# Kernel tuning notes

Hardware: AMD Instinct MI355X
Metric: run time of the kernel (lower is better)

Reference implementation:

```python
import jax, jax.numpy as jnp
import numpy as np

B, T, F, D, H, L = 4, 1024, 128, 512, 8, 4
DFF = 4 * D
NE, MD = 16, 20
HD = D // H
SCALE = 1.0 / HD ** 0.5


def _ln(x, w, b):
    m = jnp.mean(x, axis=-1, keepdims=True)
    v = jnp.mean((x - m) ** 2, axis=-1, keepdims=True)
    return (x - m) * jax.lax.rsqrt(v + 1e-5) * w + b


def setup_inputs() -> dict:
    key = jax.random.key(0)
    ks = jax.random.split(key, 16)
    rn = lambda k, shape: jax.random.normal(k, shape, jnp.float32) * 0.02
    return {
        'node_features': jax.random.normal(ks[0], (B, T, F), jnp.float32),
        'centrality': jax.random.uniform(ks[1], (B, T), jnp.float32),
        'edge_types': jax.random.randint(ks[2], (B, T, T), 0, NE),
        'sp_dist': jax.random.randint(ks[3], (B, T, T), 0, MD + 1),
        'node_W': rn(ks[4], (F, D)), 'node_b': jnp.zeros((D,), jnp.float32),
        'cent_W': rn(ks[5], (D,)), 'cent_b': jnp.zeros((D,), jnp.float32),
        'edge_emb': rn(ks[6], (NE, H)), 'dist_emb': rn(ks[7], (MD + 1, H)),
        'ln1_w': jnp.ones((L, D), jnp.float32), 'ln1_b': jnp.zeros((L, D), jnp.float32),
        'q_W': rn(ks[8], (L, D, D)), 'q_b': jnp.zeros((L, D), jnp.float32),
        'k_W': rn(ks[9], (L, D, D)), 'k_b': jnp.zeros((L, D), jnp.float32),
        'v_W': rn(ks[10], (L, D, D)), 'v_b': jnp.zeros((L, D), jnp.float32),
        'o_W': rn(ks[11], (L, D, D)), 'o_b': jnp.zeros((L, D), jnp.float32),
        'ln2_w': jnp.ones((L, D), jnp.float32), 'ln2_b': jnp.zeros((L, D), jnp.float32),
        'f1_W': rn(ks[12], (L, D, DFF)), 'f1_b': jnp.zeros((L, DFF), jnp.float32),
        'f2_W': rn(ks[13], (L, DFF, D)), 'f2_b': jnp.zeros((L, D), jnp.float32),
    }


def _forward(node_features, centrality, edge_types, sp_dist,
             node_W, node_b, cent_W, cent_b, edge_emb, dist_emb,
             ln1_w, ln1_b, q_W, q_b, k_W, k_b, v_W, v_b, o_W, o_b,
             ln2_w, ln2_b, f1_W, f1_b, f2_W, f2_b):
    # node embedding + centrality encoding
    h = node_features @ node_W + node_b                      # [B,T,D]
    h = h + centrality[..., None] * cent_W + cent_b          # Linear(1,D)
    # Graphormer attention bias: [B,T,T,H] -> [B,H,T,T]
    sp = jnp.clip(sp_dist, 0, MD)
    attn_bias = (edge_emb[edge_types] + dist_emb[sp]).transpose(0, 3, 1, 2)

    def step(h, p):
        l1w, l1b, qW, qb, kW, kb, vW, vb, oW, ob, l2w, l2b, w1, b1, w2, b2 = p
        x = _ln(h, l1w, l1b)
        q = (x @ qW + qb).reshape(B, T, H, HD)
        k = (x @ kW + kb).reshape(B, T, H, HD)
        v = (x @ vW + vb).reshape(B, T, H, HD)
        scores = jnp.einsum('bihd,bjhd->bhij', q, k) * SCALE + attn_bias
        attn = jax.nn.softmax(scores, axis=-1)
        o = jnp.einsum('bhij,bjhd->bihd', attn, v).reshape(B, T, D)
        h = h + (o @ oW + ob)                                # dropout in eval mode
        x2 = _ln(h, l2w, l2b)
        h = h + (jax.nn.silu(x2 @ w1 + b1) @ w2 + b2)
        return h, None

    layer_params = (ln1_w, ln1_b, q_W, q_b, k_W, k_b, v_W, v_b, o_W, o_b,
                    ln2_w, ln2_b, f1_W, f1_b, f2_W, f2_b)
    h, _ = jax.lax.scan(step, h, layer_params)
    return h


def reference(node_features, centrality, edge_types, sp_dist,
              node_W, node_b, cent_W, cent_b, edge_emb, dist_emb,
              ln1_w, ln1_b, q_W, q_b, k_W, k_b, v_W, v_b, o_W, o_b,
              ln2_w, ln2_b, f1_W, f1_b, f2_W, f2_b):
    return _forward(node_features, centrality, edge_types, sp_dist,
                    node_W, node_b, cent_W, cent_b, edge_emb, dist_emb,
                    ln1_w, ln1_b, q_W, q_b, k_W, k_b, v_W, v_b, o_W, o_b,
                    ln2_w, ln2_b, f1_W, f1_b, f2_W, f2_b)
```

## Files before the change

kernel.cpp:

```cpp
#include <hip/hip_runtime.h>
#include <cstddef>
#include <cstdint>

#define B_    4
#define T_    1024
#define F_    128
#define D_    512
#define H_    8
#define L_    4
#define DFF_  2048
#define HD_   64
#define SCALE_ 0.125f

typedef __attribute__((ext_vector_type(8))) short bf16x8;
typedef __attribute__((ext_vector_type(4))) float f32x4;

#define AS1(p) ((const __attribute__((address_space(1))) void*)(p))
#define AS3(p) ((__attribute__((address_space(3))) void*)(p))

__device__ __forceinline__ short f2bf(float f) {
    unsigned u = __float_as_uint(f);
    u += 0x7FFFu + ((u >> 16) & 1u);
    return (short)(u >> 16);
}

__global__ __launch_bounds__(256) void cast_nf_k(
    const float* __restrict__ src, short* __restrict__ dst)
{
    const int i = (blockIdx.x * 256 + threadIdx.x) << 2;
    const float4 v = *(const float4*)(src + i);
    short4 o = make_short4(f2bf(v.x), f2bf(v.y), f2bf(v.z), f2bf(v.w));
    *(short4*)(dst + i) = o;
}

__global__ __launch_bounds__(256) void ln_k(
    const float* __restrict__ X, const float* __restrict__ w,
    const float* __restrict__ b, short* __restrict__ Y)
{
    const int row = blockIdx.x;
    const int tid = threadIdx.x;
    const float* xr = X + (size_t)row * D_;
    const float v0 = xr[tid];
    const float v1 = xr[tid + 256];
    float s  = v0 + v1;
    float s2 = v0 * v0 + v1 * v1;
#pragma unroll
    for (int off = 1; off < 64; off <<= 1) {
        s  += __shfl_xor(s,  off);
        s2 += __shfl_xor(s2, off);
    }
    __shared__ float ss[4], ss2[4];
    if ((tid & 63) == 0) { ss[tid >> 6] = s; ss2[tid >> 6] = s2; }
    __syncthreads();
    s  = ss[0]  + ss[1]  + ss[2]  + ss[3];
    s2 = ss2[0] + ss2[1] + ss2[2] + ss2[3];
    const float mean = s * (1.f / D_);
    const float var  = s2 * (1.f / D_) - mean * mean;
    const float r    = rsqrtf(var + 1e-5f);
    short* yr = Y + (size_t)row * D_;
    yr[tid]       = f2bf((v0 - mean) * r * w[tid]       + b[tid]);
    yr[tid + 256] = f2bf((v1 - mean) * r * w[tid + 256] + b[tid + 256]);
}

__global__ __launch_bounds__(256) void transpose_all_k(
    const float* __restrict__ qW, const float* __restrict__ kW,
    const float* __restrict__ vW, const float* __restrict__ oW,
    const float* __restrict__ f1W, const float* __restrict__ f2W,
    const float* __restrict__ nW,
    short* __restrict__ WqkvT, short* __restrict__ WoT,
    short* __restrict__ Wf1T, short* __restrict__ Wf2T,
    short* __restrict__ nWt)
{
    const int id = blockIdx.y;
    const float* src; short* dst; int K, N;
    if (id < 12) {
        const int l = id / 3, which = id % 3;
        const float* s3 = (which == 0) ? qW : (which == 1) ? kW : vW;
        src = s3 + (size_t)l * D_ * D_;
        dst = WqkvT + ((size_t)l * 3 + which) * D_ * D_;
        K = D_; N = D_;
    } else if (id < 16) {
        const int l = id - 12;
        src = oW + (size_t)l * D_ * D_;  dst = WoT + (size_t)l * D_ * D_;
        K = D_; N = D_;
    } else if (id < 20) {
        const int l = id - 16;
        src = f1W + (size_t)l * D_ * DFF_;  dst = Wf1T + (size_t)l * DFF_ * D_;
        K = D_; N = DFF_;
    } else if (id < 24) {
        const int l = id - 20;
        src = f2W + (size_t)l * DFF_ * D_;  dst = Wf2T + (size_t)l * D_ * DFF_;
        K = DFF_; N = D_;
    } else {
        src = nW; dst = nWt; K = F_; N = D_;
    }
    const int ntiles = (K >> 5) * (N >> 5);
    if ((int)blockIdx.x >= ntiles) return;
    const int nt = N >> 5;
    const int k0 = (blockIdx.x / nt) << 5, n0 = (blockIdx.x % nt) << 5;

    __shared__ float t[32][33];
    const int c = threadIdx.x, r0 = threadIdx.y;
#pragma unroll
    for (int i = 0; i < 32; i += 8)
        t[r0 + i][c] = src[(size_t)(k0 + r0 + i) * N + n0 + c];
    __syncthreads();
#pragma unroll
    for (int i = 0; i < 32; i += 8)
        dst[(size_t)(n0 + r0 + i) * K + k0 + c] = f2bf(t[c][r0 + i]);
}

__global__ __launch_bounds__(256) void fuse_bias_k(
    const float* __restrict__ qb, const float* __restrict__ kb,
    const float* __restrict__ vb, float* __restrict__ dst)
{
    const int i = blockIdx.x * 256 + threadIdx.x;
    const int l = i / 1536, c = i % 1536;
    float v;
    if (c < 512)       v = qb[l * 512 + c];
    else if (c < 1024) v = kb[l * 512 + c - 512];
    else               v = vb[l * 512 + c - 1024];
    dst[i] = v;
}

__global__ __launch_bounds__(256) void bias_k(
    const int* __restrict__ et, const int* __restrict__ sp,
    const float* __restrict__ ee, const float* __restrict__ de,
    short* __restrict__ biasT)
{
    __shared__ float eeS[16][8], deS[21][8];
    const int tid = threadIdx.x;
    if (tid < 128) eeS[tid >> 3][tid & 7] = ee[tid];
    for (int t = tid; t < 168; t += 256)
        deS[t >> 3][t & 7] = de[t];
    __syncthreads();
    const int gid = blockIdx.x * 256 + tid;
    const int j4  = (gid & 255) << 2;
    const int bi  = gid >> 8;
    const size_t base = (size_t)bi * T_ + j4;
    const int4 e = *(const int4*)(et + base);
    const int4 s = *(const int4*)(sp + base);
    const int b = bi >> 10, i = bi & 1023;
    const int ex[4] = {e.x, e.y, e.z, e.w};
    const int sx[4] = {min(s.x, 20), min(s.y, 20), min(s.z, 20), min(s.w, 20)};
#pragma unroll
    for (int h = 0; h < 8; ++h) {
        short4 o;
        o.x = f2bf(eeS[ex[0]][h] + deS[sx[0]][h]);
        o.y = f2bf(eeS[ex[1]][h] + deS[sx[1]][h]);
        o.z = f2bf(eeS[ex[2]][h] + deS[sx[2]][h]);
        o.w = f2bf(eeS[ex[3]][h] + deS[sx[3]][h]);
        *(short4*)(biasT + ((size_t)((b * H_ + h) * T_ + i)) * T_ + j4) = o;
    }
}

__global__ __launch_bounds__(256) void embed_mm_k(
    const short* __restrict__ A, const short* __restrict__ Wt,
    const float* __restrict__ nb, const float* __restrict__ cb,
    const float* __restrict__ cW, const float* __restrict__ cent,
    float* __restrict__ C)
{
    const int K = F_, N = D_;
    __shared__ short As[128 * 32];
    __shared__ short Bs[64 * 32];
    const int tid  = threadIdx.x;
    const int lane = tid & 63, wv = tid >> 6;
    const int bm = blockIdx.y << 7, bn = blockIdx.x << 6;
    const int wm = (wv & 1) << 6, wn = (wv >> 1) << 5;

    const int c0 = (wv << 6) + lane;
    const int m0 = c0 >> 2, q0 = (c0 & 3) ^ ((m0 >> 1) & 3);
    const int c1 = 256 + c0;
    const int m1 = c1 >> 2, q1 = (c1 & 3) ^ ((m1 >> 1) & 3);

    const short* gA0 = A  + (size_t)(bm + m0) * K + (q0 << 3);
    const short* gA1 = A  + (size_t)(bm + m1) * K + (q1 << 3);
    const short* gB0 = Wt + (size_t)(bn + m0) * K + (q0 << 3);

    f32x4 acc[4][2];
#pragma unroll
    for (int i = 0; i < 4; ++i)
#pragma unroll
        for (int j = 0; j < 2; ++j)
            acc[i][j] = (f32x4){0.f, 0.f, 0.f, 0.f};

    const int fm = lane & 15, fq = lane >> 4;
    int caddr[4], baddr[2];
#pragma unroll
    for (int t = 0; t < 4; ++t) {
        const int rowA = wm + (t << 4) + fm;
        caddr[t] = ((rowA << 2) + (fq ^ ((rowA >> 1) & 3))) << 3;
    }
#pragma unroll
    for (int t = 0; t < 2; ++t) {
        const int rowB = wn + (t << 4) + fm;
        baddr[t] = ((rowB << 2) + (fq ^ ((rowB >> 1) & 3))) << 3;
    }

    for (int k0 = 0; k0 < K; k0 += 32) {
        __builtin_amdgcn_global_load_lds(AS1(gA0), AS3(As + (wv << 9)),        16, 0, 0);
        __builtin_amdgcn_global_load_lds(AS1(gA1), AS3(As + 2048 + (wv << 9)), 16, 0, 0);
        __builtin_amdgcn_global_load_lds(AS1(gB0), AS3(Bs + (wv << 9)),        16, 0, 0);
        gA0 += 32; gA1 += 32; gB0 += 32;
        __syncthreads();

        bf16x8 af[4], bf[2];
#pragma unroll
        for (int t = 0; t < 4; ++t) af[t] = *(const bf16x8*)(As + caddr[t]);
#pragma unroll
        for (int t = 0; t < 2; ++t) bf[t] = *(const bf16x8*)(Bs + baddr[t]);
#pragma unroll
        for (int i = 0; i < 4; ++i)
#pragma unroll
            for (int j = 0; j < 2; ++j)
                acc[i][j] = __builtin_amdgcn_mfma_f32_16x16x32_bf16(
                    af[i], bf[j], acc[i][j], 0, 0, 0);
        __syncthreads();
    }

    const int col0 = bn + wn + fm;
    const int row0 = bm + wm + (fq << 2);
#pragma unroll
    for (int j = 0; j < 2; ++j) {
        const int colg = col0 + (j << 4);
        const float bb = nb[colg] + cb[colg];
        const float cw = cW[colg];
#pragma unroll
        for (int i = 0; i < 4; ++i) {
#pragma unroll
            for (int r = 0; r < 4; ++r) {
                const int rowg = row0 + (i << 4) + r;
                C[(size_t)rowg * N + colg] = acc[i][j][r] + bb + cent[rowg] * cw;
            }
        }
    }
}

template <int OUTM, int ACT, int RES>
__global__ __launch_bounds__(256) void mm_k(
    const short* __restrict__ A, const short* __restrict__ Wt,
    const float* __restrict__ bias, const float* __restrict__ R,
    void* __restrict__ Cv, short* __restrict__ VtOut, int M, int N, int K)
{
    __shared__ short As[128 * 32];
    __shared__ short Bs[128 * 32];
    const int tid  = threadIdx.x;
    const int lane = tid & 63, wv = tid >> 6;
    const int bm = blockIdx.y << 7, bn = blockIdx.x << 7;
    const int wm = (wv & 1) << 6, wn = (wv >> 1) << 6;

    const int c0 = (wv << 6) + lane;
    const int m0 = c0 >> 2, q0 = (c0 & 3) ^ ((m0 >> 1) & 3);
    const int c1 = 256 + c0;
    const int m1 = c1 >> 2, q1 = (c1 & 3) ^ ((m1 >> 1) & 3);

    const short* gA0 = A  + (size_t)(bm + m0) * K + (q0 << 3);
    const short* gA1 = A  + (size_t)(bm + m1) * K + (q1 << 3);
    const short* gB0 = Wt + (size_t)(bn + m0) * K + (q0 << 3);
    const short* gB1 = Wt + (size_t)(bn + m1) * K + (q1 << 3);

    f32x4 acc[4][4];
#pragma unroll
    for (int i = 0; i < 4; ++i)
#pragma unroll
        for (int j = 0; j < 4; ++j)
            acc[i][j] = (f32x4){0.f, 0.f, 0.f, 0.f};

    const int fm = lane & 15, fq = lane >> 4;
    int caddr[4], baddr[4];
#pragma unroll
    for (int t = 0; t < 4; ++t) {
        const int rowA = wm + (t << 4) + fm;
        caddr[t] = ((rowA << 2) + (fq ^ ((rowA >> 1) & 3))) << 3;
        const int rowB = wn + (t << 4) + fm;
        baddr[t] = ((rowB << 2) + (fq ^ ((rowB >> 1) & 3))) << 3;
    }

    for (int k0 = 0; k0 < K; k0 += 32) {
        __builtin_amdgcn_global_load_lds(AS1(gA0), AS3(As + (wv << 9)),        16, 0, 0);
        __builtin_amdgcn_global_load_lds(AS1(gA1), AS3(As + 2048 + (wv << 9)), 16, 0, 0);
        __builtin_amdgcn_global_load_lds(AS1(gB0), AS3(Bs + (wv << 9)),        16, 0, 0);
        __builtin_amdgcn_global_load_lds(AS1(gB1), AS3(Bs + 2048 + (wv << 9)), 16, 0, 0);
        gA0 += 32; gA1 += 32; gB0 += 32; gB1 += 32;
        __syncthreads();

        bf16x8 af[4], bf[4];
#pragma unroll
        for (int t = 0; t < 4; ++t) {
            af[t] = *(const bf16x8*)(As + caddr[t]);
            bf[t] = *(const bf16x8*)(Bs + baddr[t]);
        }
#pragma unroll
        for (int i = 0; i < 4; ++i)
#pragma unroll
            for (int j = 0; j < 4; ++j)
                acc[i][j] = __builtin_amdgcn_mfma_f32_16x16x32_bf16(
                    af[i], bf[j], acc[i][j], 0, 0, 0);
        __syncthreads();
    }

    const int col0 = bn + wn + fm;
    const int row0 = bm + wm + (fq << 2);
    float* Cf = (float*)Cv;
    short* Cb = (short*)Cv;
#pragma unroll
    for (int j = 0; j < 4; ++j) {
        const int colg = col0 + (j << 4);
        const float bb = bias[colg];
#pragma unroll
        for (int i = 0; i < 4; ++i) {
#pragma unroll
            for (int r = 0; r < 4; ++r) {
                const int rowg = row0 + (i << 4) + r;
                float v = acc[i][j][r] + bb;
                if (ACT) v = v / (1.f + __expf(-v));
                if (OUTM == 2) {
                    if (colg < 1024) {
                        Cb[(size_t)rowg * 1024 + colg] = f2bf(v);
                    } else {
                        const int da = colg - 1024;
                        const int hh = da >> 6, dd = da & 63;
                        const int bb2 = rowg >> 10, tt = rowg & 1023;
                        VtOut[((size_t)(bb2 * H_ + hh) * 64 + dd) * T_ + tt] = f2bf(v);
                    }
                } else {
                    const size_t off = (size_t)rowg * N + colg;
                    if (RES) v += R[off];
                    if (OUTM == 1) Cb[off] = f2bf(v);
                    else           Cf[off] = v;
                }
            }
        }
    }
}

__global__ __launch_bounds__(256) void mm64_k(
    const short* __restrict__ A, const short* __restrict__ Wt,
    const float* __restrict__ bias, const float* __restrict__ R,
    float* __restrict__ C, int M, int N, int K)
{
    __shared__ short As[128 * 32];
    __shared__ short Bs[64 * 32];
    const int tid  = threadIdx.x;
    const int lane = tid & 63, wv = tid >> 6;
    const int bm = blockIdx.y << 7, bn = blockIdx.x << 6;
    const int wm = (wv & 1) << 6, wn = (wv >> 1) << 5;

    const int c0 = (wv << 6) + lane;
    const int m0 = c0 >> 2, q0 = (c0 & 3) ^ ((m0 >> 1) & 3);
    const int c1 = 256 + c0;
    const int m1 = c1 >> 2, q1 = (c1 & 3) ^ ((m1 >> 1) & 3);

    const short* gA0 = A  + (size_t)(bm + m0) * K + (q0 << 3);
    const short* gA1 = A  + (size_t)(bm + m1) * K + (q1 << 3);
    const short* gB0 = Wt + (size_t)(bn + m0) * K + (q0 << 3);

    f32x4 acc[4][2];
#pragma unroll
    for (int i = 0; i < 4; ++i)
#pragma unroll
        for (int j = 0; j < 2; ++j)
            acc[i][j] = (f32x4){0.f, 0.f, 0.f, 0.f};

    const int fm = lane & 15, fq = lane >> 4;
    int caddr[4], baddr[2];
#pragma unroll
    for (int t = 0; t < 4; ++t) {
        const int rowA = wm + (t << 4) + fm;
        caddr[t] = ((rowA << 2) + (fq ^ ((rowA >> 1) & 3))) << 3;
    }
#pragma unroll
    for (int t = 0; t < 2; ++t) {
        const int rowB = wn + (t << 4) + fm;
        baddr[t] = ((rowB << 2) + (fq ^ ((rowB >> 1) & 3))) << 3;
    }

    for (int k0 = 0; k0 < K; k0 += 32) {
        __builtin_amdgcn_global_load_lds(AS1(gA0), AS3(As + (wv << 9)),        16, 0, 0);
        __builtin_amdgcn_global_load_lds(AS1(gA1), AS3(As + 2048 + (wv << 9)), 16, 0, 0);
        __builtin_amdgcn_global_load_lds(AS1(gB0), AS3(Bs + (wv << 9)),        16, 0, 0);
        gA0 += 32; gA1 += 32; gB0 += 32;
        __syncthreads();

        bf16x8 af[4], bf[2];
#pragma unroll
        for (int t = 0; t < 4; ++t) af[t] = *(const bf16x8*)(As + caddr[t]);
#pragma unroll
        for (int t = 0; t < 2; ++t) bf[t] = *(const bf16x8*)(Bs + baddr[t]);
#pragma unroll
        for (int i = 0; i < 4; ++i)
#pragma unroll
            for (int j = 0; j < 2; ++j)
                acc[i][j] = __builtin_amdgcn_mfma_f32_16x16x32_bf16(
                    af[i], bf[j], acc[i][j], 0, 0, 0);
        __syncthreads();
    }

    const int col0 = bn + wn + fm;
    const int row0 = bm + wm + (fq << 2);
#pragma unroll
    for (int j = 0; j < 2; ++j) {
        const int colg = col0 + (j << 4);
        const float bb = bias[colg];
#pragma unroll
        for (int i = 0; i < 4; ++i) {
#pragma unroll
            for (int r = 0; r < 4; ++r) {
                const int rowg = row0 + (i << 4) + r;
                const size_t off = (size_t)rowg * N + colg;
                C[off] = acc[i][j][r] + bb + R[off];
            }
        }
    }
}

__global__ __launch_bounds__(256) void flash_k(
    const short* __restrict__ QKb, const short* __restrict__ Vt,
    const short* __restrict__ biasT, short* __restrict__ O)
{
    const int tid = threadIdx.x;
    const int i0 = blockIdx.x << 6;
    const int h  = blockIdx.y;
    const int b  = blockIdx.z;
    const int lane = tid & 63, w = tid >> 6;
    const int fm = lane & 15, q = lane >> 4;

    __shared__ short Ks[4096];
    __shared__ short Vs[4096];
    __shared__ short Ps[64][72];

    const short* qp = QKb + (size_t)(b * T_ + i0 + (w << 4) + fm) * 1024 + (h << 6) + (q << 3);
    const bf16x8 aq0 = *(const bf16x8*)(qp);
    const bf16x8 aq1 = *(const bf16x8*)(qp + 32);

    const int s0 = (w << 6) + lane, r0 = s0 >> 3, cc0 = (s0 & 7) ^ (r0 & 7);
    const int s1 = 256 + s0,        r1 = s1 >> 3, cc1 = (s1 & 7) ^ (r1 & 7);
    const short* gK0 = QKb + (size_t)(b * T_ + r0) * 1024 + 512 + (h << 6) + (cc0 << 3);
    const short* gK1 = QKb + (size_t)(b * T_ + r1) * 1024 + 512 + (h << 6) + (cc1 << 3);
    const short* gV0 = Vt + ((size_t)((b * H_ + h) << 6) + r0) * T_ + (cc0 << 3);
    const short* gV1 = Vt + ((size_t)((b * H_ + h) << 6) + r1) * T_ + (cc1 << 3);

    int fAddr[4][2];
#pragma unroll
    for (int t = 0; t < 4; ++t) {
        const int row = (t << 4) + fm;
#pragma unroll
        for (int ks = 0; ks < 2; ++ks)
            fAddr[t][ks] = (row << 6) + (((q + (ks << 2)) ^ (row & 7)) << 3);
    }

    const short* bptr = biasT +
        ((size_t)(b * H_ + h) * T_ + i0 + (w << 4) + (q << 2)) * T_ + fm;

    f32x4 accO[4];
#pragma unroll
    for (int dt = 0; dt < 4; ++dt) accO[dt] = (f32x4){0.f, 0.f, 0.f, 0.f};
    float m_i[4] = {-1e30f, -1e30f, -1e30f, -1e30f};
    float l_i[4] = {0.f, 0.f, 0.f, 0.f};

    const int irow = b * T_ + i0 + (w << 4) + (q << 2);
    short* psW = &Ps[(w << 4) + (q << 2)][fm];
    const short* psR = &Ps[(w << 4) + fm][q << 3];

    for (int j0 = 0; j0 < T_; j0 += 64) {
        __syncthreads();
        __builtin_amdgcn_global_load_lds(AS1(gK0 + (size_t)j0 * 1024), AS3(Ks + (s0 << 3)), 16, 0, 0);
        __builtin_amdgcn_global_load_lds(AS1(gK1 + (size_t)j0 * 1024), AS3(Ks + (s1 << 3)), 16, 0, 0);
        __builtin_amdgcn_global_load_lds(AS1(gV0 + j0), AS3(Vs + (s0 << 3)), 16, 0, 0);
        __builtin_amdgcn_global_load_lds(AS1(gV1 + j0), AS3(Vs + (s1 << 3)), 16, 0, 0);

        float bb[4][4];
#pragma unroll
        for (int r = 0; r < 4; ++r)
#pragma unroll
            for (int jt = 0; jt < 4; ++jt) {
                const unsigned u = *(const unsigned short*)(bptr + (size_t)r * T_ + j0 + (jt << 4));
                bb[r][jt] = __uint_as_float(u << 16);
            }
        __syncthreads();

        f32x4 s[4];
#pragma unroll
        for (int jt = 0; jt < 4; ++jt) s[jt] = (f32x4){0.f, 0.f, 0.f, 0.f};
#pragma unroll
        for (int jt = 0; jt < 4; ++jt) {
            const bf16x8 k0 = *(const bf16x8*)(Ks + fAddr[jt][0]);
            const bf16x8 k1 = *(const bf16x8*)(Ks + fAddr[jt][1]);
            s[jt] = __builtin_amdgcn_mfma_f32_16x16x32_bf16(aq0, k0, s[jt], 0, 0, 0);
            s[jt] = __builtin_amdgcn_mfma_f32_16x16x32_bf16(aq1, k1, s[jt], 0, 0, 0);
        }

        float sv[4][4];
#pragma unroll
        for (int r = 0; r < 4; ++r)
#pragma unroll
            for (int jt = 0; jt < 4; ++jt)
                sv[r][jt] = fmaf(s[jt][r], SCALE_, bb[r][jt]);

#pragma unroll
        for (int r = 0; r < 4; ++r) {
            float mx = fmaxf(fmaxf(sv[r][0], sv[r][1]), fmaxf(sv[r][2], sv[r][3]));
#pragma unroll
            for (int off = 1; off < 16; off <<= 1)
                mx = fmaxf(mx, __shfl_xor(mx, off));
            const float mnew = fmaxf(m_i[r], mx);
            const float al   = __expf(m_i[r] - mnew);
            m_i[r] = mnew;
            float rs = 0.f;
#pragma unroll
            for (int jt = 0; jt < 4; ++jt) {
                sv[r][jt] = __expf(sv[r][jt] - mnew);
                rs += sv[r][jt];
            }
#pragma unroll
            for (int off = 1; off < 16; off <<= 1) rs += __shfl_xor(rs, off);
            l_i[r] = l_i[r] * al + rs;
#pragma unroll
            for (int dt = 0; dt < 4; ++dt) accO[dt][r] *= al;
        }

#pragma unroll
        for (int r = 0; r < 4; ++r)
#pragma unroll
            for (int jt = 0; jt < 4; ++jt)
                psW[(size_t)r * 72 + (jt << 4)] = f2bf(sv[r][jt]);

#pragma unroll
        for (int ks = 0; ks < 2; ++ks) {
            const bf16x8 ap = *(const bf16x8*)(psR + (ks << 5));
#pragma unroll
            for (int dt = 0; dt < 4; ++dt) {
                const bf16x8 bv = *(const bf16x8*)(Vs + fAddr[dt][ks]);
                accO[dt] = __builtin_amdgcn_mfma_f32_16x16x32_bf16(ap, bv, accO[dt], 0, 0, 0);
            }
        }
    }

#pragma unroll
    for (int r = 0; r < 4; ++r) {
        const float inv = 1.f / l_i[r];
        short* op = O + (size_t)(irow + r) * D_ + (h << 6) + fm;
#pragma unroll
        for (int dt = 0; dt < 4; ++dt)
            op[dt << 4] = f2bf(accO[dt][r] * inv);
    }
}

extern "C" void kernel_launch(void* const* d_in, const int* in_sizes, int n_in,
                              void* d_out, int out_size, void* d_ws, size_t ws_size,
                              hipStream_t stream)
{
    (void)in_sizes; (void)n_in; (void)out_size; (void)ws_size;

    const float* nf   = (const float*)d_in[0];
    const float* cent = (const float*)d_in[1];
    const int*   et   = (const int*)  d_in[2];
    const int*   sp   = (const int*)  d_in[3];
    const float* nW   = (const float*)d_in[4];
    const float* nb   = (const float*)d_in[5];
    const float* cW   = (const float*)d_in[6];
    const float* cb   = (const float*)d_in[7];
    const float* ee   = (const float*)d_in[8];
    const float* de   = (const float*)d_in[9];
    const float* ln1w = (const float*)d_in[10];
    const float* ln1b = (const float*)d_in[11];
    const float* qW   = (const float*)d_in[12];
    const float* qb   = (const float*)d_in[13];
    const float* kW   = (const float*)d_in[14];
    const float* kb   = (const float*)d_in[15];
    const float* vW   = (const float*)d_in[16];
    const float* vb   = (const float*)d_in[17];
    const float* oW   = (const float*)d_in[18];
    const float* ob   = (const float*)d_in[19];
    const float* ln2w = (const float*)d_in[20];
    const float* ln2b = (const float*)d_in[21];
    const float* f1W  = (const float*)d_in[22];
    const float* f1b  = (const float*)d_in[23];
    const float* f2W  = (const float*)d_in[24];
    const float* f2b  = (const float*)d_in[25];

    const int M = B_ * T_;
    char* p = (char*)d_ws;
    float* Hbuf  = (float*)p;  p += (size_t)M * D_ * 4;
    short* QKb   = (short*)p;  p += (size_t)M * 1024 * 2;
    short* Vt    = (short*)p;  p += (size_t)B_ * H_ * 64 * T_ * 2;
    float* biasf = (float*)p;  p += (size_t)L_ * 3 * D_ * 4;
    short* Xbuf  = (short*)p;  p += (size_t)M * D_ * 2;
    short* Ob    = (short*)p;  p += (size_t)M * D_ * 2;
    short* FF    = (short*)p;  p += (size_t)M * DFF_ * 2;
    short* biasT = (short*)p;  p += (size_t)B_ * H_ * T_ * T_ * 2;
    short* WqkvT = (short*)p;  p += (size_t)L_ * 3 * D_ * D_ * 2;
    short* WoT   = (short*)p;  p += (size_t)L_ * D_ * D_ * 2;
    short* Wf1T  = (short*)p;  p += (size_t)L_ * DFF_ * D_ * 2;
    short* Wf2T  = (short*)p;  p += (size_t)L_ * D_ * DFF_ * 2;
    short* nfb   = (short*)p;  p += (size_t)M * F_ * 2;
    short* nWt   = (short*)p;  p += (size_t)D_ * F_ * 2;

    float* out = (float*)d_out;

    transpose_all_k<<<dim3(1024, 25), dim3(32, 8), 0, stream>>>(
        qW, kW, vW, oW, f1W, f2W, nW, WqkvT, WoT, Wf1T, Wf2T, nWt);
    cast_nf_k<<<dim3(M * F_ / 1024), dim3(256), 0, stream>>>(nf, nfb);
    fuse_bias_k<<<dim3(L_ * 3 * D_ / 256), dim3(256), 0, stream>>>(qb, kb, vb, biasf);
    bias_k<<<dim3(B_ * T_ * T_ / 1024), dim3(256), 0, stream>>>(et, sp, ee, de, biasT);
    embed_mm_k<<<dim3(D_ / 64, M / 128), dim3(256), 0, stream>>>(
        nfb, nWt, nb, cb, cW, cent, Hbuf);

    const dim3 blk(256);
    const dim3 gQKV(3 * D_ / 128, M / 128);
    const dim3 gO64(D_ / 64,      M / 128);
    const dim3 gF1 (DFF_ / 128,   M / 128);
    const dim3 gAttn(T_ / 64, H_, B_);

    for (int l = 0; l < L_; ++l) {
        const size_t bOff  = (size_t)l * D_;
        const size_t b1Off = (size_t)l * DFF_;

        ln_k<<<dim3(M), blk, 0, stream>>>(Hbuf, ln1w + bOff, ln1b + bOff, Xbuf);

        mm_k<2, 0, 0><<<gQKV, blk, 0, stream>>>(
            Xbuf, WqkvT + (size_t)l * 3 * D_ * D_, biasf + (size_t)l * 3 * D_,
            nullptr, QKb, Vt, M, 3 * D_, D_);

        flash_k<<<gAttn, blk, 0, stream>>>(QKb, Vt, biasT, Ob);

        mm64_k<<<gO64, blk, 0, stream>>>(
            Ob, WoT + (size_t)l * D_ * D_, ob + bOff, Hbuf, Hbuf, M, D_, D_);

        ln_k<<<dim3(M), blk, 0, stream>>>(Hbuf, ln2w + bOff, ln2b + bOff, Xbuf);

        mm_k<1, 1, 0><<<gF1, blk, 0, stream>>>(
            Xbuf, Wf1T + (size_t)l * DFF_ * D_, f1b + b1Off, nullptr, FF, nullptr, M, DFF_, D_);

        float* cdst = (l == L_ - 1) ? out : Hbuf;
        mm64_k<<<gO64, blk, 0, stream>>>(
            FF, Wf2T + (size_t)l * D_ * DFF_, f2b + bOff, Hbuf, cdst, M, D_, DFF_);
    }
}
```

Measured before the change: 748.4 us.

## Drop online softmax max tracking, split KV across two blocks with combine

```diff
diff --git a/kernel.cpp b/kernel.cpp
--- a/kernel.cpp
+++ b/kernel.cpp
@@ -11,6 +11,8 @@
 #define DFF_  2048
 #define HD_   64
 #define SCALE_ 0.125f
+#define LOG2E_ 1.4426950408889634f
+#define CL2E_  (SCALE_ * LOG2E_)
 
 typedef __attribute__((ext_vector_type(8))) short bf16x8;
 typedef __attribute__((ext_vector_type(4))) float f32x4;
@@ -146,10 +148,10 @@
 #pragma unroll
     for (int h = 0; h < 8; ++h) {
         short4 o;
-        o.x = f2bf(eeS[ex[0]][h] + deS[sx[0]][h]);
-        o.y = f2bf(eeS[ex[1]][h] + deS[sx[1]][h]);
-        o.z = f2bf(eeS[ex[2]][h] + deS[sx[2]][h]);
-        o.w = f2bf(eeS[ex[3]][h] + deS[sx[3]][h]);
+        o.x = f2bf((eeS[ex[0]][h] + deS[sx[0]][h]) * LOG2E_);
+        o.y = f2bf((eeS[ex[1]][h] + deS[sx[1]][h]) * LOG2E_);
+        o.z = f2bf((eeS[ex[2]][h] + deS[sx[2]][h]) * LOG2E_);
+        o.w = f2bf((eeS[ex[3]][h] + deS[sx[3]][h]) * LOG2E_);
         *(short4*)(biasT + ((size_t)((b * H_ + h) * T_ + i)) * T_ + j4) = o;
     }
 }
@@ -416,10 +418,13 @@
 
 __global__ __launch_bounds__(256) void flash_k(
     const short* __restrict__ QKb, const short* __restrict__ Vt,
-    const short* __restrict__ biasT, short* __restrict__ O)
+    const short* __restrict__ biasT, float* __restrict__ Opart,
+    float* __restrict__ Lpart)
 {
     const int tid = threadIdx.x;
-    const int i0 = blockIdx.x << 6;
+    const int bx = blockIdx.x;
+    const int it = bx >> 1, split = bx & 1;
+    const int i0 = it << 6;
     const int h  = blockIdx.y;
     const int b  = blockIdx.z;
     const int lane = tid & 63, w = tid >> 6;
@@ -452,17 +457,20 @@
     const short* bptr = biasT +
         ((size_t)(b * H_ + h) * T_ + i0 + (w << 4) + (q << 2)) * T_ + fm;
 
+    const short oneb = 0x3F80;
+    const bf16x8 ones = {oneb, oneb, oneb, oneb, oneb, oneb, oneb, oneb};
+
     f32x4 accO[4];
 #pragma unroll
     for (int dt = 0; dt < 4; ++dt) accO[dt] = (f32x4){0.f, 0.f, 0.f, 0.f};
-    float m_i[4] = {-1e30f, -1e30f, -1e30f, -1e30f};
-    float l_i[4] = {0.f, 0.f, 0.f, 0.f};
+    f32x4 accL = (f32x4){0.f, 0.f, 0.f, 0.f};
 
     const int irow = b * T_ + i0 + (w << 4) + (q << 2);
     short* psW = &Ps[(w << 4) + (q << 2)][fm];
     const short* psR = &Ps[(w << 4) + fm][q << 3];
 
-    for (int j0 = 0; j0 < T_; j0 += 64) {
+    const int jbeg = split << 9, jend = jbeg + 512;
+    for (int j0 = jbeg; j0 < jend; j0 += 64) {
         __syncthreads();
         __builtin_amdgcn_global_load_lds(AS1(gK0 + (size_t)j0 * 1024), AS3(Ks + (s0 << 3)), 16, 0, 0);
         __builtin_amdgcn_global_load_lds(AS1(gK1 + (size_t)j0 * 1024), AS3(Ks + (s1 << 3)), 16, 0, 0);
@@ -490,44 +498,18 @@
             s[jt] = __builtin_amdgcn_mfma_f32_16x16x32_bf16(aq1, k1, s[jt], 0, 0, 0);
         }
 
-        float sv[4][4];
 #pragma unroll
         for (int r = 0; r < 4; ++r)
 #pragma unroll
-            for (int jt = 0; jt < 4; ++jt)
-                sv[r][jt] = fmaf(s[jt][r], SCALE_, bb[r][jt]);
-
-#pragma unroll
-        for (int r = 0; r < 4; ++r) {
-            float mx = fmaxf(fmaxf(sv[r][0], sv[r][1]), fmaxf(sv[r][2], sv[r][3]));
-#pragma unroll
-            for (int off = 1; off < 16; off <<= 1)
-                mx = fmaxf(mx, __shfl_xor(mx, off));
-            const float mnew = fmaxf(m_i[r], mx);
-            const float al   = __expf(m_i[r] - mnew);
-            m_i[r] = mnew;
-            float rs = 0.f;
-#pragma unroll
             for (int jt = 0; jt < 4; ++jt) {
-                sv[r][jt] = __expf(sv[r][jt] - mnew);
-                rs += sv[r][jt];
+                const float p = __builtin_amdgcn_exp2f(fmaf(s[jt][r], CL2E_, bb[r][jt]));
+                psW[(size_t)r * 72 + (jt << 4)] = f2bf(p);
             }
-#pragma unroll
-            for (int off = 1; off < 16; off <<= 1) rs += __shfl_xor(rs, off);
-            l_i[r] = l_i[r] * al + rs;
-#pragma unroll
-            for (int dt = 0; dt < 4; ++dt) accO[dt][r] *= al;
-        }
-
-#pragma unroll
-        for (int r = 0; r < 4; ++r)
-#pragma unroll
-            for (int jt = 0; jt < 4; ++jt)
-                psW[(size_t)r * 72 + (jt << 4)] = f2bf(sv[r][jt]);
 
 #pragma unroll
         for (int ks = 0; ks < 2; ++ks) {
             const bf16x8 ap = *(const bf16x8*)(psR + (ks << 5));
+            accL = __builtin_amdgcn_mfma_f32_16x16x32_bf16(ap, ones, accL, 0, 0, 0);
 #pragma unroll
             for (int dt = 0; dt < 4; ++dt) {
                 const bf16x8 bv = *(const bf16x8*)(Vs + fAddr[dt][ks]);
@@ -536,14 +518,38 @@
         }
     }
 
+    float* obase = Opart + (size_t)split * B_ * T_ * D_;
 #pragma unroll
     for (int r = 0; r < 4; ++r) {
-        const float inv = 1.f / l_i[r];
-        short* op = O + (size_t)(irow + r) * D_ + (h << 6) + fm;
+        float* op = obase + (size_t)(irow + r) * D_ + (h << 6) + fm;
 #pragma unroll
         for (int dt = 0; dt < 4; ++dt)
-            op[dt << 4] = f2bf(accO[dt][r] * inv);
-    }
+            op[dt << 4] = accO[dt][r];
+    }
+    if (fm == 0) {
+#pragma unroll
+        for (int r = 0; r < 4; ++r)
+            Lpart[(size_t)split * B_ * T_ * H_ + (size_t)(irow + r) * H_ + h] = accL[r];
+    }
+}
+
+__global__ __launch_bounds__(256) void combine_k(
+    const float* __restrict__ Opart, const float* __restrict__ Lpart,
+    short* __restrict__ Ob)
+{
+    const int gid = blockIdx.x * 256 + threadIdx.x;
+    const int d4  = (gid & 127) << 2;
+    const int row = gid >> 7;
+    const int h   = d4 >> 6;
+    const float l = Lpart[(size_t)row * H_ + h] +
+                    Lpart[(size_t)B_ * T_ * H_ + (size_t)row * H_ + h];
+    const float inv = 1.f / l;
+    const size_t o = (size_t)row * D_ + d4;
+    const float4 a = *(const float4*)(Opart + o);
+    const float4 c = *(const float4*)(Opart + (size_t)B_ * T_ * D_ + o);
+    short4 r = make_short4(f2bf((a.x + c.x) * inv), f2bf((a.y + c.y) * inv),
+                           f2bf((a.z + c.z) * inv), f2bf((a.w + c.w) * inv));
+    *(short4*)(Ob + o) = r;
 }
 
 extern "C" void kernel_launch(void* const* d_in, const int* in_sizes, int n_in,
@@ -595,6 +601,8 @@
     short* Wf2T  = (short*)p;  p += (size_t)L_ * D_ * DFF_ * 2;
     short* nfb   = (short*)p;  p += (size_t)M * F_ * 2;
     short* nWt   = (short*)p;  p += (size_t)D_ * F_ * 2;
+    float* Opart = (float*)p;  p += (size_t)2 * M * D_ * 4;
+    float* Lpart = (float*)p;  p += (size_t)2 * M * H_ * 4;
 
     float* out = (float*)d_out;
 
@@ -610,7 +618,8 @@
     const dim3 gQKV(3 * D_ / 128, M / 128);
     const dim3 gO64(D_ / 64,      M / 128);
     const dim3 gF1 (DFF_ / 128,   M / 128);
-    const dim3 gAttn(T_ / 64, H_, B_);
+    const dim3 gAttn(2 * T_ / 64, H_, B_);
+    const dim3 gCmb(M * D_ / 1024);
 
     for (int l = 0; l < L_; ++l) {
         const size_t bOff  = (size_t)l * D_;
@@ -622,7 +631,8 @@
             Xbuf, WqkvT + (size_t)l * 3 * D_ * D_, biasf + (size_t)l * 3 * D_,
             nullptr, QKb, Vt, M, 3 * D_, D_);
 
-        flash_k<<<gAttn, blk, 0, stream>>>(QKb, Vt, biasT, Ob);
+        flash_k<<<gAttn, blk, 0, stream>>>(QKb, Vt, biasT, Opart, Lpart);
+        combine_k<<<gCmb, blk, 0, stream>>>(Opart, Lpart, Ob);
 
         mm64_k<<<gO64, blk, 0, stream>>>(
             Ob, WoT + (size_t)l * D_ * D_, ob + bOff, Hbuf, Hbuf, M, D_, D_);
```

Result: faster. 701.0 us (-6.3%).
